# Kernel tuning notes

Hardware: AMD Instinct MI355X
Metric: run time of the kernel (lower is better)

## Reference

```python
import jax, jax.numpy as jnp
import numpy as np

B, T, D, H, K = 128, 128, 2048, 512, 512
KSIZES = (2, 3, 4, 5)
OUT_DIM = 2048
IN_DIM = 2 * H + len(KSIZES) * K + D  # 5120
BN_EPS = 1e-5


def _gru_dir(x, w_ih, w_hh, b_ih, b_hh):
    """Single-direction torch-style GRU. x: [B,T,D] -> [B,T,H]."""
    xw = jnp.einsum('btd,gd->btg', x, w_ih) + b_ih  # precompute input proj [B,T,3H]
    h0 = jnp.zeros((x.shape[0], w_hh.shape[1]), x.dtype)

    def step(h, xw_t):
        gh = h @ w_hh.T + b_hh
        xr, xz, xn = jnp.split(xw_t, 3, axis=-1)
        hr, hz, hn = jnp.split(gh, 3, axis=-1)
        r = jax.nn.sigmoid(xr + hr)
        z = jax.nn.sigmoid(xz + hz)
        n = jnp.tanh(xn + r * hn)
        h_new = (1.0 - z) * n + z * h
        return h_new, h_new

    _, hs = jax.lax.scan(step, h0, jnp.swapaxes(xw, 0, 1))
    return jnp.swapaxes(hs, 0, 1)


def _forward(videos, videos_origin, videos_mask, lengths,
             w_ih_f, w_hh_f, b_ih_f, b_hh_f,
             w_ih_b, w_hh_b, b_ih_b, b_hh_b,
             conv_w2, conv_b2, conv_w3, conv_b3, conv_w4, conv_b4, conv_w5, conv_b5,
             fc_w, fc_b, bn_gamma, bn_beta, bn_mean, bn_var):
    # bidirectional GRU on the full padded sequence (torch code does NOT pack)
    fwd = _gru_dir(videos, w_ih_f, w_hh_f, b_ih_f, b_hh_f)
    bwd = _gru_dir(videos[:, ::-1], w_ih_b, w_hh_b, b_ih_b, b_hh_b)[:, ::-1]
    gru_init = jnp.concatenate([fwd, bwd], axis=-1)  # [B,T,2H]

    # fused masked mean (replaces per-sample python loop): mean over first lengths[i] steps
    masked = gru_init * videos_mask[:, :, None]
    mean_gru = masked.sum(axis=1) / lengths.astype(gru_init.dtype)[:, None]  # [B,2H]

    # multi-scale text-CNN over masked GRU outputs
    x4 = masked[:, None, :, :]  # [B,1,T,2H]
    cons = []
    for w, cw, cb in zip(KSIZES, (conv_w2, conv_w3, conv_w4, conv_w5),
                         (conv_b2, conv_b3, conv_b4, conv_b5)):
        y = jax.lax.conv_general_dilated(
            x4, cw, window_strides=(1, 1), padding=[(w - 1, w - 1), (0, 0)],
            dimension_numbers=('NCHW', 'OIHW', 'NCHW'))  # [B,K,T+w-1,1]
        y = jax.nn.relu(y + cb[None, :, None, None])
        cons.append(y.max(axis=(2, 3)))  # global max-pool over time
    con_out = jnp.concatenate(cons, axis=1)  # [B, 4K]

    # concate == 'full' ; dropout is identity at inference
    feats = jnp.concatenate([mean_gru, con_out, videos_origin], axis=1)  # [B,5120]
    feats = feats @ fc_w + fc_b
    feats = bn_gamma * (feats - bn_mean) / jnp.sqrt(bn_var + BN_EPS) + bn_beta
    # l2norm over feature dim
    feats = feats / jnp.sqrt(jnp.sum(feats * feats, axis=1, keepdims=True))
    return feats


def setup_inputs() -> dict:
    key = jax.random.key(0)
    ks = jax.random.split(key, 32)
    s = 0.02
    inp = {
        'videos': jax.random.normal(ks[0], (B, T, D), jnp.float32),
        'videos_origin': jax.random.normal(ks[1], (B, D), jnp.float32),
    }
    lengths = jax.random.randint(ks[2], (B,), 1, T + 1).astype(jnp.int64)
    inp['lengths'] = lengths
    inp['videos_mask'] = (jnp.arange(T)[None, :] < lengths[:, None]).astype(jnp.float32)
    inp['w_ih_f'] = jax.random.normal(ks[3], (3 * H, D), jnp.float32) * s
    inp['w_hh_f'] = jax.random.normal(ks[4], (3 * H, H), jnp.float32) * s
    inp['b_ih_f'] = jnp.zeros((3 * H,), jnp.float32)
    inp['b_hh_f'] = jnp.zeros((3 * H,), jnp.float32)
    inp['w_ih_b'] = jax.random.normal(ks[5], (3 * H, D), jnp.float32) * s
    inp['w_hh_b'] = jax.random.normal(ks[6], (3 * H, H), jnp.float32) * s
    inp['b_ih_b'] = jnp.zeros((3 * H,), jnp.float32)
    inp['b_hh_b'] = jnp.zeros((3 * H,), jnp.float32)
    for i, w in enumerate(KSIZES):
        inp[f'conv_w{w}'] = jax.random.normal(ks[7 + i], (K, 1, w, 2 * H), jnp.float32) * s
        inp[f'conv_b{w}'] = jnp.zeros((K,), jnp.float32)
    inp['fc_w'] = jax.random.normal(ks[12], (IN_DIM, OUT_DIM), jnp.float32) * s
    inp['fc_b'] = jnp.zeros((OUT_DIM,), jnp.float32)
    inp['bn_gamma'] = jnp.ones((OUT_DIM,), jnp.float32)
    inp['bn_beta'] = jnp.zeros((OUT_DIM,), jnp.float32)
    inp['bn_mean'] = jnp.zeros((OUT_DIM,), jnp.float32)
    inp['bn_var'] = jnp.ones((OUT_DIM,), jnp.float32)
    return inp


def reference(videos, videos_origin, lengths, videos_mask,
              w_ih_f, w_hh_f, b_ih_f, b_hh_f,
              w_ih_b, w_hh_b, b_ih_b, b_hh_b,
              conv_w2, conv_b2, conv_w3, conv_b3, conv_w4, conv_b4, conv_w5, conv_b5,
              fc_w, fc_b, bn_gamma, bn_beta, bn_mean, bn_var):
    return _forward(videos, videos_origin, videos_mask, lengths,
                    w_ih_f, w_hh_f, b_ih_f, b_hh_f,
                    w_ih_b, w_hh_b, b_ih_b, b_hh_b,
                    conv_w2, conv_b2, conv_w3, conv_b3, conv_w4, conv_b4, conv_w5, conv_b5,
                    fc_w, fc_b, bn_gamma, bn_beta, bn_mean, bn_var)
```

## Files before the change

### kernel.cpp

```cpp
#include <hip/hip_runtime.h>
#include <stdint.h>

#define B_   128
#define T_   128
#define D_   2048
#define H_   512
#define G3   1536
#define CH   1024
#define KC   512
#define OUTD 2048
#define IND  5120
#define TP   168
#define MPAD 144

typedef short vb8 __attribute__((ext_vector_type(8)));
typedef float v4f __attribute__((ext_vector_type(4)));

__device__ __forceinline__ unsigned short f2b(float f) {
  unsigned u = __float_as_uint(f);
  u = (u + 0x7FFFu + ((u >> 16) & 1u)) >> 16;
  return (unsigned short)u;
}
__device__ __forceinline__ float b2f(unsigned short u) {
  return __uint_as_float((unsigned)u << 16);
}

__device__ __forceinline__ void gl16(const unsigned short* g, unsigned short* l) {
  __builtin_amdgcn_global_load_lds(
      (const __attribute__((address_space(1))) void*)g,
      (__attribute__((address_space(3))) void*)l, 16, 0, 0);
}

__global__ void k_cvt(const float* __restrict__ in, unsigned short* __restrict__ out, int n4) {
  int stride = gridDim.x * blockDim.x;
  for (int i = blockIdx.x * blockDim.x + threadIdx.x; i < n4; i += stride) {
    float4 v = reinterpret_cast<const float4*>(in)[i];
    ushort4 o;
    o.x = f2b(v.x); o.y = f2b(v.y); o.z = f2b(v.z); o.w = f2b(v.w);
    reinterpret_cast<ushort4*>(out)[i] = o;
  }
}

__global__ void k_tcvt(const float* __restrict__ in, unsigned short* __restrict__ out) {
  __shared__ float tile[32][33];
  const int tx = threadIdx.x & 31;
  const int ty = threadIdx.x >> 5;
  const int n0 = blockIdx.x * 32;
  const int k0 = blockIdx.y * 32;
#pragma unroll
  for (int i = 0; i < 4; ++i)
    tile[ty + 8 * i][tx] = in[(size_t)(k0 + ty + 8 * i) * OUTD + n0 + tx];
  __syncthreads();
#pragma unroll
  for (int i = 0; i < 4; ++i)
    out[(size_t)(n0 + ty + 8 * i) * IND + k0 + tx] = f2b(tile[tx][ty + 8 * i]);
}

template<int EPI, int CB>
__global__ __launch_bounds__(256) void k_gemm(
    const unsigned short* __restrict__ A,
    const unsigned short* __restrict__ Bm,
    const float* __restrict__ bias,
    void* __restrict__ Cv,
    int K, int lda, int ldc, int convw)
{
  __shared__ unsigned short sA[2 * 128 * 32];
  __shared__ unsigned short sB[2 * 128 * 32];
  float*          C32 = (float*)Cv;
  unsigned short* C16 = (unsigned short*)Cv;

  const int m0 = blockIdx.x * 128;
  const int n0 = blockIdx.y * 128;
  const int cz = blockIdx.z;

  int K_ = K;
  int w_ = convw;
  int koff = 0;
  const unsigned short* Bm_ = Bm;
  const float* bias_ = bias;
  if (EPI == 1) {
    constexpr int cum[4] = {0, 2, 5, 9};
    w_   = cz + 2;
    K_   = w_ * CH;
    Bm_  = Bm + (size_t)cum[cz] * KC * CH;
    bias_ = bias + cz * KC;
  } else if (EPI == 3) {
    koff = cz * K;
  }
  const int bstride = (EPI == 3) ? convw : K_;

  const int tid  = threadIdx.x;
  const int lane = tid & 63;
  const int wv   = tid >> 6;
  const int wr   = wv >> 1;
  const int wc   = wv & 1;

  const unsigned short* ag[2];
  const unsigned short* bg[2];
  unsigned short* al[2];
  unsigned short* bl[2];
#pragma unroll
  for (int q = 0; q < 2; ++q) {
    int c  = wv * 2 + q;
    int r  = c * 16 + (lane >> 2);
    int kc = (lane & 3) * 8;
    long abase;
    if (EPI == 1) {
      int m   = m0 + r;
      int b   = m / MPAD;
      int tau = m - b * MPAD;
      abase = (long)(b * TP + 4 + tau - (w_ - 1)) * CH;
    } else {
      abase = (long)(m0 + r) * lda + koff;
    }
    ag[q] = A + abase + kc;
    bg[q] = Bm_ + (long)(n0 + r) * bstride + kc + koff;
    al[q] = sA + c * 512;
    bl[q] = sB + c * 512;
  }

  v4f acc[4][4] = {};
  const int kq = (lane >> 4) * 8;
  const int fr = lane & 15;

  for (int k0 = 0; k0 < K_; k0 += 64) {
    if (k0) __syncthreads();
#pragma unroll
    for (int q = 0; q < 2; ++q) {
      gl16(ag[q] + k0,      al[q]);
      gl16(ag[q] + k0 + 32, al[q] + 4096);
      gl16(bg[q] + k0,      bl[q]);
      gl16(bg[q] + k0 + 32, bl[q] + 4096);
    }
    __syncthreads();
#pragma unroll
    for (int kk = 0; kk < 2; ++kk) {
      const int hb = kk * 4096;
      vb8 af[4], bfr[4];
#pragma unroll
      for (int i = 0; i < 4; ++i) {
        af[i]  = *reinterpret_cast<const vb8*>(sA + hb + (wr * 64 + i * 16 + fr) * 32 + kq);
        bfr[i] = *reinterpret_cast<const vb8*>(sB + hb + (wc * 64 + i * 16 + fr) * 32 + kq);
      }
#pragma unroll
      for (int i = 0; i < 4; ++i)
#pragma unroll
        for (int j = 0; j < 4; ++j)
          acc[i][j] = __builtin_amdgcn_mfma_f32_16x16x32_bf16(af[i], bfr[j], acc[i][j], 0, 0, 0);
    }
  }

  const int rl = lane >> 4;
#pragma unroll
  for (int i = 0; i < 4; ++i) {
#pragma unroll
    for (int j = 0; j < 4; ++j) {
      int col = n0 + wc * 64 + j * 16 + fr;
      float bs = (EPI == 3) ? 0.f : bias_[col];
      if (EPI == 0) {
#pragma unroll
        for (int r = 0; r < 4; ++r) {
          int m = m0 + wr * 64 + i * 16 + rl * 4 + r;
          float v = acc[i][j][r] + bs;
          if (CB) C16[(long)m * ldc + col] = f2b(v);
          else    C32[(long)m * ldc + col] = v;
        }
      } else if (EPI == 2) {
        const int dirb = col >= G3;
        const int xcol = col - dirb * G3;
        unsigned short* base = C16 + (size_t)dirb * ((size_t)B_ * T_ * G3);
#pragma unroll
        for (int r = 0; r < 4; ++r) {
          int m = m0 + wr * 64 + i * 16 + rl * 4 + r;
          base[(long)m * G3 + xcol] = f2b(acc[i][j][r] + bs);
        }
      } else if (EPI == 3) {
#pragma unroll
        for (int r = 0; r < 4; ++r) {
          int m = m0 + wr * 64 + i * 16 + rl * 4 + r;
          C32[(size_t)cz * (B_ * OUTD) + (long)m * ldc + col] = acc[i][j][r];
        }
      } else {
        int mf = m0 + wr * 64 + i * 16;
        int b  = mf / MPAD;
        int tf = mf - b * MPAD;
        float mx = 0.f;
#pragma unroll
        for (int r = 0; r < 4; ++r) {
          int tau = tf + rl * 4 + r;
          float v = acc[i][j][r] + bs;
          v = v > 0.f ? v : 0.f;
          if (tau < T_ + w_ - 1) mx = v > mx ? v : mx;
        }
        mx = fmaxf(mx, __shfl_xor(mx, 16));
        mx = fmaxf(mx, __shfl_xor(mx, 32));
        if (rl == 0 && tf < T_ + w_ - 1)
          atomicMax(reinterpret_cast<int*>(C32 + (long)b * ldc + cz * KC + col),
                    __float_as_int(mx));
      }
    }
  }
}

__global__ __launch_bounds__(512) void k_scan(
    const unsigned short* __restrict__ whh16,
    const float* __restrict__ bhhf, const float* __restrict__ bhhb,
    const unsigned short* __restrict__ xw,
    const int* __restrict__ lengths,
    unsigned short* __restrict__ hbuf,
    unsigned short* __restrict__ xpad,
    float* __restrict__ meang,
    unsigned int* __restrict__ flags)
{
  __shared__ unsigned short sw[96 * 512];
  const int wg   = blockIdx.x;
  const int dir  = wg >> 4;
  const int u0   = (wg & 15) * 32;
  const int tid  = threadIdx.x;
  const int lane = tid & 63;
  const int wv   = tid >> 6;
  const int fr   = lane & 15;
  const int rl   = lane >> 4;
  const int kq   = rl * 8;

  const unsigned short* Wd  = whh16 + (size_t)dir * (3 * H_ * H_);
  const float*          bhh = dir ? bhhb : bhhf;
  const unsigned short* xwd = xw + (size_t)dir * ((size_t)B_ * T_ * G3);
  unsigned short* hb = hbuf + dir * (2 * B_ * H_);
  unsigned int* myflags = flags + dir * 16 * 16;

  for (int i = tid; i < 96 * 64; i += 512) {
    int row  = i >> 6;
    int slot = i & 63;
    const unsigned short* src = Wd + (size_t)((row >> 5) * H_ + u0 + (row & 31)) * H_ + slot * 8;
    *reinterpret_cast<vb8*>((char*)sw + ((row * 1024 + slot * 16) ^ ((row & 7) << 4))) =
        *reinterpret_cast<const vb8*>(src);
  }
  __syncthreads();

  int mylen[4];
#pragma unroll
  for (int r = 0; r < 4; ++r) mylen[r] = lengths[wv * 16 + rl * 4 + r];

  float bh[3][2];
#pragma unroll
  for (int g = 0; g < 3; ++g)
#pragma unroll
    for (int j = 0; j < 2; ++j) bh[g][j] = bhh[g * H_ + u0 + j * 16 + fr];

  float hst[8], macc[8];
#pragma unroll
  for (int i = 0; i < 8; ++i) { hst[i] = 0.f; macc[i] = 0.f; }

  unsigned short uxw[3][2][4];
  {
    const int t0 = dir ? (T_ - 1) : 0;
#pragma unroll
    for (int g = 0; g < 3; ++g)
#pragma unroll
      for (int j = 0; j < 2; ++j)
#pragma unroll
        for (int r = 0; r < 4; ++r)
          uxw[g][j][r] = xwd[((size_t)(wv * 16 + rl * 4 + r) * T_ + t0) * G3 +
                             g * H_ + u0 + j * 16 + fr];
  }

  for (int s = 0; s < T_; ++s) {
    const int t = dir ? (T_ - 1 - s) : s;

    v4f acc[3][2] = {};
    if (s > 0) {
      const unsigned short* arow = hb + ((s - 1) & 1) * (B_ * H_) + (wv * 16 + fr) * H_;
#pragma unroll 4
      for (int ks = 0; ks < 16; ++ks) {
        vb8 a = *reinterpret_cast<const vb8*>(arow + ks * 32 + kq);
#pragma unroll
        for (int g = 0; g < 3; ++g)
#pragma unroll
          for (int j = 0; j < 2; ++j) {
            vb8 wf = *reinterpret_cast<const vb8*>(
                (const char*)sw +
                (((g * 32 + j * 16 + fr) * 1024 + ks * 64 + rl * 16) ^ ((fr & 7) << 4)));
            acc[g][j] = __builtin_amdgcn_mfma_f32_16x16x32_bf16(a, wf, acc[g][j], 0, 0, 0);
          }
      }
    }

    unsigned short* hc = hb + (s & 1) * (B_ * H_);
#pragma unroll
    for (int j = 0; j < 2; ++j)
#pragma unroll
      for (int r = 0; r < 4; ++r) {
        const int idx = j * 4 + r;
        const int b   = wv * 16 + rl * 4 + r;
        const int u   = u0 + j * 16 + fr;
        float xr = b2f(uxw[0][j][r]), xz = b2f(uxw[1][j][r]), xn = b2f(uxw[2][j][r]);
        float hr = acc[0][j][r] + bh[0][j];
        float hz = acc[1][j][r] + bh[1][j];
        float hn = acc[2][j][r] + bh[2][j];
        float rr = 1.f / (1.f + __expf(-(xr + hr)));
        float z  = 1.f / (1.f + __expf(-(xz + hz)));
        float ax = xn + rr * hn;
        float n  = 2.f / (1.f + __expf(-2.f * ax)) - 1.f;
        float h  = (1.f - z) * n + z * hst[idx];
        hst[idx] = h;
        hc[b * H_ + u] = f2b(h);
        if (t < mylen[r]) {
          xpad[((size_t)b * TP + 4 + t) * CH + dir * H_ + u] = f2b(h);
          macc[idx] += h;
        }
      }

    if (s < T_ - 1) {
      const int tn = dir ? (T_ - 2 - s) : (s + 1);
#pragma unroll
      for (int g = 0; g < 3; ++g)
#pragma unroll
        for (int j = 0; j < 2; ++j)
#pragma unroll
          for (int r = 0; r < 4; ++r)
            uxw[g][j][r] = xwd[((size_t)(wv * 16 + rl * 4 + r) * T_ + tn) * G3 +
                               g * H_ + u0 + j * 16 + fr];
      __syncthreads();
      if (tid == 0) {
        __builtin_amdgcn_fence(__ATOMIC_RELEASE, "agent");
        __hip_atomic_store(&myflags[(wg & 15) * 16], (unsigned)(s + 1),
                           __ATOMIC_RELAXED, __HIP_MEMORY_SCOPE_AGENT);
      }
      if (tid < 16) {
        while (__hip_atomic_load(&myflags[tid * 16], __ATOMIC_RELAXED,
                                 __HIP_MEMORY_SCOPE_AGENT) < (unsigned)(s + 1))
          __builtin_amdgcn_s_sleep(1);
      }
      if (tid == 0)
        __builtin_amdgcn_fence(__ATOMIC_ACQUIRE, "agent");
      __syncthreads();
    }
  }

#pragma unroll
  for (int j = 0; j < 2; ++j)
#pragma unroll
    for (int r = 0; r < 4; ++r)
      meang[(size_t)(wv * 16 + rl * 4 + r) * CH + dir * H_ + u0 + j * 16 + fr] =
          macc[j * 4 + r] / (float)mylen[r];
}

__global__ void k_feats(const float* __restrict__ mg, const float* __restrict__ co,
                        const float* __restrict__ vo, unsigned short* __restrict__ out) {
  int i = blockIdx.x * 256 + threadIdx.x;
  int b = i / IND, c = i - b * IND;
  float v;
  if (c < CH) v = mg[b * CH + c];
  else if (c < CH + OUTD) v = co[b * OUTD + (c - CH)];
  else v = vo[b * D_ + (c - CH - OUTD)];
  out[i] = f2b(v);
}

__global__ __launch_bounds__(256) void k_bnnorm(const float* __restrict__ x,
    const float* __restrict__ fcb,
    const float* __restrict__ g, const float* __restrict__ bt,
    const float* __restrict__ mn, const float* __restrict__ vr,
    float* __restrict__ out) {
  const int b = blockIdx.x;
  const size_t PL = (size_t)B_ * OUTD;
  __shared__ float red[4];
  float vals[8];
  float ss = 0.f;
#pragma unroll
  for (int i = 0; i < 8; ++i) {
    int c = threadIdx.x + i * 256;
    size_t o = (size_t)b * OUTD + c;
    float xs = x[o] + x[PL + o] + x[2 * PL + o] + x[3 * PL + o] + fcb[c];
    float y = g[c] * (xs - mn[c]) / sqrtf(vr[c] + 1e-5f) + bt[c];
    vals[i] = y;
    ss += y * y;
  }
#pragma unroll
  for (int s2 = 1; s2 < 64; s2 <<= 1) ss += __shfl_xor(ss, s2);
  if ((threadIdx.x & 63) == 0) red[threadIdx.x >> 6] = ss;
  __syncthreads();
  float inv = 1.f / sqrtf(red[0] + red[1] + red[2] + red[3]);
#pragma unroll
  for (int i = 0; i < 8; ++i)
    out[(size_t)b * OUTD + threadIdx.x + i * 256] = vals[i] * inv;
}

extern "C" void kernel_launch(void* const* d_in, const int* in_sizes, int n_in,
                              void* d_out, int out_size, void* d_ws, size_t ws_size,
                              hipStream_t stream) {
  (void)in_sizes; (void)n_in; (void)out_size; (void)ws_size;
  const float* videos = (const float*)d_in[0];
  const float* vorig  = (const float*)d_in[1];
  const int*   lens   = (const int*)d_in[2];
  const float* wihf = (const float*)d_in[4];
  const float* whhf = (const float*)d_in[5];
  const float* bihf = (const float*)d_in[6];
  const float* bhhf = (const float*)d_in[7];
  const float* wihb = (const float*)d_in[8];
  const float* whhb = (const float*)d_in[9];
  const float* bihb = (const float*)d_in[10];
  const float* bhhb = (const float*)d_in[11];
  const float* cw[4] = {(const float*)d_in[12], (const float*)d_in[14],
                        (const float*)d_in[16], (const float*)d_in[18]};
  const float* cb[4] = {(const float*)d_in[13], (const float*)d_in[15],
                        (const float*)d_in[17], (const float*)d_in[19]};
  const float* fcw = (const float*)d_in[20];
  const float* fcb = (const float*)d_in[21];
  const float* bng = (const float*)d_in[22];
  const float* bnb = (const float*)d_in[23];
  const float* bnm = (const float*)d_in[24];
  const float* bnv = (const float*)d_in[25];
  float* out = (float*)d_out;

  char* ws = (char*)d_ws;
  size_t off = 0;
  auto alloc = [&](size_t bytes) -> void* {
    void* p = ws + off;
    off = (off + bytes + 255) & ~(size_t)255;
    return p;
  };
  unsigned int*   flags  = (unsigned int*)alloc(4096);
  unsigned short* xw16   = (unsigned short*)alloc((size_t)2 * B_ * T_ * G3 * 2);
  unsigned short* whh16  = (unsigned short*)alloc((size_t)2 * 3 * H_ * H_ * 2);
  unsigned short* hbuf   = (unsigned short*)alloc((size_t)2 * 2 * B_ * H_ * 2);
  float*          meang  = (float*)alloc((size_t)B_ * CH * 4);
  float*          conout = (float*)alloc((size_t)B_ * OUTD * 4);
  unsigned short* feats  = (unsigned short*)alloc((size_t)B_ * IND * 2);
  float*          fcpart = (float*)alloc((size_t)4 * B_ * OUTD * 4);
  unsigned short* wihcat = (unsigned short*)alloc((size_t)2 * G3 * D_ * 2);
  unsigned short* cw16   = (unsigned short*)alloc((size_t)KC * 14 * CH * 2);
  unsigned short* vid16  = (unsigned short*)alloc((size_t)B_ * T_ * D_ * 2);
  float*          biascat= (float*)alloc(2 * G3 * 4);
  float*          cbcat  = (float*)alloc(4 * KC * 4);
  unsigned short* xpad = vid16;
  unsigned short* fcT  = vid16 + (size_t)B_ * TP * CH;

  hipMemsetAsync(flags, 0, 4096, stream);
  hipMemsetAsync(conout, 0, (size_t)B_ * OUTD * 4, stream);
  hipMemcpyAsync(biascat,      bihf, G3 * 4, hipMemcpyDeviceToDevice, stream);
  hipMemcpyAsync(biascat + G3, bihb, G3 * 4, hipMemcpyDeviceToDevice, stream);
  for (int i = 0; i < 4; ++i)
    hipMemcpyAsync(cbcat + i * KC, cb[i], KC * 4, hipMemcpyDeviceToDevice, stream);

  k_cvt<<<2048, 256, 0, stream>>>(videos, vid16, B_ * T_ * D_ / 4);
  k_cvt<<<512, 256, 0, stream>>>(wihf, wihcat, G3 * D_ / 4);
  k_cvt<<<512, 256, 0, stream>>>(wihb, wihcat + (size_t)G3 * D_, G3 * D_ / 4);
  k_cvt<<<768, 256, 0, stream>>>(whhf, whh16, 3 * H_ * H_ / 4);
  k_cvt<<<768, 256, 0, stream>>>(whhb, whh16 + (size_t)3 * H_ * H_, 3 * H_ * H_ / 4);
  {
    size_t cwoff = 0;
    for (int i = 0; i < 4; ++i) {
      int w = i + 2;
      int n = KC * w * CH;
      k_cvt<<<256, 256, 0, stream>>>(cw[i], cw16 + cwoff, n / 4);
      cwoff += (size_t)n;
    }
  }

  k_gemm<2, 1><<<dim3(128, 24), 256, 0, stream>>>(vid16, wihcat, biascat, xw16, D_, D_, 0, 0);

  hipMemsetAsync(xpad, 0, (size_t)B_ * TP * CH * 2, stream);
  k_tcvt<<<dim3(64, 160), 256, 0, stream>>>(fcw, fcT);

  k_scan<<<dim3(32), dim3(512), 0, stream>>>(whh16, bhhf, bhhb, xw16, lens,
                                             hbuf, xpad, meang, flags);

  k_gemm<1, 0><<<dim3(144, 4, 4), 256, 0, stream>>>(xpad, cw16, cbcat, conout, 0, 0, OUTD, 0);

  k_feats<<<2560, 256, 0, stream>>>(meang, conout, vorig, feats);
  k_gemm<3, 0><<<dim3(1, 16, 4), 256, 0, stream>>>(feats, fcT, fcb, fcpart,
                                                   IND / 4, IND, OUTD, IND);
  k_bnnorm<<<B_, 256, 0, stream>>>(fcpart, fcb, bng, bnb, bnm, bnv, out);
}
```

Baseline: 1.757 ms.

## Retile GRU scan waves to 32 batch rows by 16 units, precompute offsets

Each of the 8 waves in the recurrent scan kernel now covers 32 batch rows and 16 hidden units instead of 16 rows and 32 units. Each weight fragment read from LDS then feeds two MFMAs, cutting LDS weight traffic per step, at the cost of two global h-row loads per k-step. Per-element global offsets for xw, the h buffer and xpad are also precomputed once and advanced incrementally, removing per-step index arithmetic from the serial loop. This raises register use for the offset arrays.

```diff
diff --git a/kernel.cpp b/kernel.cpp
--- a/kernel.cpp
+++ b/kernel.cpp
@@ -219,6 +219,8 @@
   const int tid  = threadIdx.x;
   const int lane = tid & 63;
   const int wv   = tid >> 6;
+  const int mg   = wv & 3;
+  const int jh   = wv >> 2;
   const int fr   = lane & 15;
   const int rl   = lane >> 4;
   const int kq   = rl * 8;
@@ -238,89 +240,111 @@
   }
   __syncthreads();
 
-  int mylen[4];
-#pragma unroll
-  for (int r = 0; r < 4; ++r) mylen[r] = lengths[wv * 16 + rl * 4 + r];
-
-  float bh[3][2];
+  const int u  = u0 + jh * 16 + fr;
+  const int t0 = dir ? (T_ - 1) : 0;
+  const int xstep = dir ? -G3 : G3;
+  const int pstep = dir ? -CH : CH;
+
+  int mylen[8];
+  int hoff[8], poff[8];
+#pragma unroll
+  for (int mt = 0; mt < 2; ++mt)
+#pragma unroll
+    for (int r = 0; r < 4; ++r) {
+      const int idx = mt * 4 + r;
+      const int b   = mg * 32 + mt * 16 + rl * 4 + r;
+      mylen[idx] = lengths[b];
+      hoff[idx]  = b * H_ + u;
+      poff[idx]  = (b * TP + 4 + t0) * CH + dir * H_ + u;
+    }
+
+  int xoff[3][2][4];
 #pragma unroll
   for (int g = 0; g < 3; ++g)
 #pragma unroll
-    for (int j = 0; j < 2; ++j) bh[g][j] = bhh[g * H_ + u0 + j * 16 + fr];
+    for (int mt = 0; mt < 2; ++mt)
+#pragma unroll
+      for (int r = 0; r < 4; ++r) {
+        const int b = mg * 32 + mt * 16 + rl * 4 + r;
+        xoff[g][mt][r] = (b * T_ + t0) * G3 + g * H_ + u;
+      }
+
+  int ab[2];
+#pragma unroll
+  for (int mt = 0; mt < 2; ++mt) ab[mt] = (mg * 32 + mt * 16 + fr) * H_ + kq;
+
+  float bh[3];
+#pragma unroll
+  for (int g = 0; g < 3; ++g) bh[g] = bhh[g * H_ + u];
 
   float hst[8], macc[8];
 #pragma unroll
   for (int i = 0; i < 8; ++i) { hst[i] = 0.f; macc[i] = 0.f; }
 
   unsigned short uxw[3][2][4];
-  {
-    const int t0 = dir ? (T_ - 1) : 0;
-#pragma unroll
-    for (int g = 0; g < 3; ++g)
-#pragma unroll
-      for (int j = 0; j < 2; ++j)
-#pragma unroll
-        for (int r = 0; r < 4; ++r)
-          uxw[g][j][r] = xwd[((size_t)(wv * 16 + rl * 4 + r) * T_ + t0) * G3 +
-                             g * H_ + u0 + j * 16 + fr];
-  }
+#pragma unroll
+  for (int g = 0; g < 3; ++g)
+#pragma unroll
+    for (int mt = 0; mt < 2; ++mt)
+#pragma unroll
+      for (int r = 0; r < 4; ++r)
+        uxw[g][mt][r] = xwd[xoff[g][mt][r]];
 
   for (int s = 0; s < T_; ++s) {
     const int t = dir ? (T_ - 1 - s) : s;
 
-    v4f acc[3][2] = {};
+    v4f acc[2][3] = {};
     if (s > 0) {
-      const unsigned short* arow = hb + ((s - 1) & 1) * (B_ * H_) + (wv * 16 + fr) * H_;
+      const unsigned short* hp = hb + ((s - 1) & 1) * (B_ * H_);
 #pragma unroll 4
       for (int ks = 0; ks < 16; ++ks) {
-        vb8 a = *reinterpret_cast<const vb8*>(arow + ks * 32 + kq);
-#pragma unroll
-        for (int g = 0; g < 3; ++g)
-#pragma unroll
-          for (int j = 0; j < 2; ++j) {
-            vb8 wf = *reinterpret_cast<const vb8*>(
-                (const char*)sw +
-                (((g * 32 + j * 16 + fr) * 1024 + ks * 64 + rl * 16) ^ ((fr & 7) << 4)));
-            acc[g][j] = __builtin_amdgcn_mfma_f32_16x16x32_bf16(a, wf, acc[g][j], 0, 0, 0);
-          }
+        vb8 a0 = *reinterpret_cast<const vb8*>(hp + ab[0] + ks * 32);
+        vb8 a1 = *reinterpret_cast<const vb8*>(hp + ab[1] + ks * 32);
+#pragma unroll
+        for (int g = 0; g < 3; ++g) {
+          const int row = g * 32 + jh * 16 + fr;
+          vb8 wf = *reinterpret_cast<const vb8*>(
+              (const char*)sw + (((row * 1024) + ks * 64 + rl * 16) ^ ((row & 7) << 4)));
+          acc[0][g] = __builtin_amdgcn_mfma_f32_16x16x32_bf16(a0, wf, acc[0][g], 0, 0, 0);
+          acc[1][g] = __builtin_amdgcn_mfma_f32_16x16x32_bf16(a1, wf, acc[1][g], 0, 0, 0);
+        }
       }
     }
 
     unsigned short* hc = hb + (s & 1) * (B_ * H_);
 #pragma unroll
-    for (int j = 0; j < 2; ++j)
+    for (int mt = 0; mt < 2; ++mt)
 #pragma unroll
       for (int r = 0; r < 4; ++r) {
-        const int idx = j * 4 + r;
-        const int b   = wv * 16 + rl * 4 + r;
-        const int u   = u0 + j * 16 + fr;
-        float xr = b2f(uxw[0][j][r]), xz = b2f(uxw[1][j][r]), xn = b2f(uxw[2][j][r]);
-        float hr = acc[0][j][r] + bh[0][j];
-        float hz = acc[1][j][r] + bh[1][j];
-        float hn = acc[2][j][r] + bh[2][j];
+        const int idx = mt * 4 + r;
+        float xr = b2f(uxw[0][mt][r]), xz = b2f(uxw[1][mt][r]), xn = b2f(uxw[2][mt][r]);
+        float hr = acc[mt][0][r] + bh[0];
+        float hz = acc[mt][1][r] + bh[1];
+        float hn = acc[mt][2][r] + bh[2];
         float rr = 1.f / (1.f + __expf(-(xr + hr)));
         float z  = 1.f / (1.f + __expf(-(xz + hz)));
         float ax = xn + rr * hn;
         float n  = 2.f / (1.f + __expf(-2.f * ax)) - 1.f;
         float h  = (1.f - z) * n + z * hst[idx];
         hst[idx] = h;
-        hc[b * H_ + u] = f2b(h);
-        if (t < mylen[r]) {
-          xpad[((size_t)b * TP + 4 + t) * CH + dir * H_ + u] = f2b(h);
+        hc[hoff[idx]] = f2b(h);
+        if (t < mylen[idx]) {
+          xpad[poff[idx]] = f2b(h);
           macc[idx] += h;
         }
+        poff[idx] += pstep;
       }
 
     if (s < T_ - 1) {
-      const int tn = dir ? (T_ - 2 - s) : (s + 1);
 #pragma unroll
       for (int g = 0; g < 3; ++g)
 #pragma unroll
-        for (int j = 0; j < 2; ++j)
-#pragma unroll
-          for (int r = 0; r < 4; ++r)
-            uxw[g][j][r] = xwd[((size_t)(wv * 16 + rl * 4 + r) * T_ + tn) * G3 +
-                               g * H_ + u0 + j * 16 + fr];
+        for (int mt = 0; mt < 2; ++mt)
+#pragma unroll
+          for (int r = 0; r < 4; ++r) {
+            xoff[g][mt][r] += xstep;
+            uxw[g][mt][r] = xwd[xoff[g][mt][r]];
+          }
       __syncthreads();
       if (tid == 0) {
         __builtin_amdgcn_fence(__ATOMIC_RELEASE, "agent");
@@ -339,11 +363,13 @@
   }
 
 #pragma unroll
-  for (int j = 0; j < 2; ++j)
-#pragma unroll
-    for (int r = 0; r < 4; ++r)
-      meang[(size_t)(wv * 16 + rl * 4 + r) * CH + dir * H_ + u0 + j * 16 + fr] =
-          macc[j * 4 + r] / (float)mylen[r];
+  for (int mt = 0; mt < 2; ++mt)
+#pragma unroll
+    for (int r = 0; r < 4; ++r) {
+      const int idx = mt * 4 + r;
+      const int b   = mg * 32 + mt * 16 + rl * 4 + r;
+      meang[(size_t)b * CH + dir * H_ + u] = macc[idx] / (float)mylen[idx];
+    }
 }
 
 __global__ void k_feats(const float* __restrict__ mg, const float* __restrict__ co,
```

Result: slower. 2.199 ms (+25.1%).
